# Kernel optimization log

Measured on AMD Instinct MI355X. Metric: run time of the kernel, lower is better.

## Reference

```python
import jax, jax.numpy as jnp
import numpy as np

N = 50000   # nodes
E = 600000  # edges (time_feat is per-edge: same mask indexes k and src_idx)
D = 128     # adapter_dim
C = 8       # num_clusters
SCALE = D ** -0.5


def setup_inputs() -> dict:
    key = jax.random.key(0)
    ks = jax.random.split(key, 12)
    s = 1.0 / np.sqrt(D)
    return {
        "node_feat": jax.random.normal(ks[0], (N, D), jnp.float32),
        "time_feat": jax.random.normal(ks[1], (E, D), jnp.float32),
        "context_feat": jax.random.normal(ks[2], (N, D), jnp.float32),
        "edge_index": jax.random.randint(ks[3], (2, E), 0, N),
        "Wq": jax.random.uniform(ks[4], (D, D), jnp.float32, -s, s),
        "bq": jnp.zeros((D,), jnp.float32),
        "Wk": jax.random.uniform(ks[5], (D, D), jnp.float32, -s, s),
        "bk": jnp.zeros((D,), jnp.float32),
        "Wv": jax.random.uniform(ks[6], (D, D), jnp.float32, -s, s),
        "bv": jnp.zeros((D,), jnp.float32),
        "cluster_emb": jax.random.normal(ks[7], (C, D), jnp.float32),
        "Wo": jax.random.uniform(ks[8], (D, D), jnp.float32, -s, s),
        "bo": jnp.zeros((D,), jnp.float32),
    }


def reference(node_feat, time_feat, context_feat, edge_index,
              Wq, bq, Wk, bk, Wv, bv, cluster_emb, Wo, bo):
    q = node_feat @ Wq + bq            # [N, D]
    k = time_feat @ Wk + bk            # [E, D]
    v = time_feat @ Wv + bv            # [E, D]

    # cluster routing: argmax(softmax(sim)) == argmax(sim)
    sim = (time_feat @ cluster_emb.T) * SCALE   # [E, C]
    assign = jnp.argmax(sim, axis=-1)           # [E] int

    src = edge_index[0]                          # [E]
    seg = assign * N + src                       # combined (cluster, dst-of-scatter) segment id
    nseg = C * N

    attn = jnp.sum(q[src] * k, axis=-1) * SCALE  # [E]

    # scatter_softmax per (cluster, src node)
    seg_max = jax.ops.segment_max(attn, seg, num_segments=nseg)
    ex = jnp.exp(attn - seg_max[seg])
    denom = jax.ops.segment_sum(ex, seg, num_segments=nseg)
    w = ex / denom[seg]                          # [E]

    # scatter_mean per (cluster, src node) -> [C, N, D]
    wv = v * w[:, None]
    sums = jax.ops.segment_sum(wv, seg, num_segments=nseg)                 # [C*N, D]
    counts = jax.ops.segment_sum(jnp.ones((E,), v.dtype), seg, num_segments=nseg)
    means = sums / jnp.maximum(counts, 1.0)[:, None]                       # empty -> 0
    per_cluster = means.reshape(C, N, D)

    # sum(outputs) / len(outputs): only non-empty clusters contribute an entry
    edges_per_cluster = jax.ops.segment_sum(jnp.ones((E,), jnp.float32), assign, num_segments=C)
    num_nonempty = jnp.sum((edges_per_cluster > 0).astype(jnp.float32))
    combined = per_cluster.sum(axis=0) / num_nonempty                      # [N, D]

    return jax.nn.relu(combined @ Wo + bo)
```

## Files before the change

kernel.cpp:

```cpp
#include <hip/hip_runtime.h>
#include <math.h>


#define NN 50000
#define NE 600000
#define DD 128
#define NC 8
#define WIN 64
#define NWIN 9376
#define NBF  9377
#define EC 60
#define NLOC 32
#define SCALEF 0.08838834764831845f

#define OFF_NODECNT  0
#define OFF_FILL     50000
#define OFF_MASK     100000
#define ZERO_ELEMS   100256
#define OFF_NODEOFF  100352
#define OFF_PARTIAL  150352
#define OFF_BF       150608
#define OFF_BQK      160000
#define OFF_BVO      160128
#define OFF_WQBK     160256
#define OFF_C0       160384
#define OFF_WQK      160400
#define OFF_WVO      176784
#define OFF_QB       193168
#define OFF_SORTED   243168
#define OFF_SRCS     843168
#define OFF_SW       1443168
#define OFF_P        1493168

__global__ __launch_bounds__(256) void k_pre_count(
    const float* __restrict__ Wq, const float* __restrict__ bq,
    const float* __restrict__ Wk, const float* __restrict__ bk,
    const float* __restrict__ Wv, const float* __restrict__ bv,
    const float* __restrict__ Wo, const int* __restrict__ ei,
    int* __restrict__ node_cnt,
    float* __restrict__ Wqk, float* __restrict__ bqk,
    float* __restrict__ Wvo, float* __restrict__ bvo,
    float* __restrict__ wqbk, float* __restrict__ c0) {
  int bid = blockIdx.x, t = threadIdx.x;
  if (bid >= 129) {
    long e = (long)(bid - 129) * 256 + t;
    if (e < NE) atomicAdd(&node_cnt[ei[e]], 1);
    return;
  }
  __shared__ float rq[DD], rv[DD];
  int b = bid;
  if (b < DD) {
    if (t < DD) { rq[t] = Wq[b * DD + t]; rv[t] = Wv[b * DD + t]; }
    __syncthreads();
    if (t < DD) {
      float aq = 0.f, av = 0.f;
      for (int j = 0; j < DD; j++) {
        aq += rq[j] * Wk[t * DD + j];
        av += rv[j] * Wo[j * DD + t];
      }
      Wqk[b * DD + t] = aq;
      Wvo[b * DD + t] = av;
    }
  } else {
    if (t < DD) {
      float a1 = 0.f, a2 = 0.f, a3 = 0.f;
      for (int j = 0; j < DD; j++) {
        a1 += bq[j] * Wk[t * DD + j];
        a2 += bv[j] * Wo[j * DD + t];
        a3 += Wq[t * DD + j] * bk[j];
      }
      bqk[t] = a1; bvo[t] = a2; wqbk[t] = a3;
      if (t == 0) {
        float s = 0.f;
        for (int j = 0; j < DD; j++) s += bq[j] * bk[j];
        *c0 = s;
      }
    }
  }
}

__global__ __launch_bounds__(256) void k_p(
    const float* __restrict__ nf, const float* __restrict__ Wqk,
    const float* __restrict__ bqk, const float* __restrict__ wqbk,
    const float* __restrict__ c0p,
    float* __restrict__ p, float* __restrict__ qb) {
  __shared__ float a_lds[64 * DD];
  __shared__ float wb_lds[DD];
  int t = threadIdx.x;
  long row0 = (long)blockIdx.x * 64;
  for (int it = 0; it < 8; it++) {
    int idx = (it * 256 + t) * 4;
    long r = row0 + idx / DD;
    float4 v = {0.f, 0.f, 0.f, 0.f};
    if (r < NN) v = *(const float4*)(nf + r * DD + (idx % DD));
    *(float4*)(a_lds + idx) = v;
  }
  if (t < DD) wb_lds[t] = wqbk[t];
  __syncthreads();
  int cg = t % 32, rg = t / 32;
  int col0 = cg * 4, r0 = rg * 8;
  float acc[8][4]; float qacc[8];
  for (int r = 0; r < 8; r++) { qacc[r] = 0.f; for (int c = 0; c < 4; c++) acc[r][c] = 0.f; }
  for (int k = 0; k < DD; k++) {
    float4 b4 = *(const float4*)(Wqk + k * DD + col0);
    float wbk = wb_lds[k];
    for (int r = 0; r < 8; r++) {
      float a = a_lds[(r0 + r) * DD + k];
      acc[r][0] += a * b4.x; acc[r][1] += a * b4.y;
      acc[r][2] += a * b4.z; acc[r][3] += a * b4.w;
      qacc[r] += a * wbk;
    }
  }
  float4 bq4 = *(const float4*)(bqk + col0);
  float c0v = *c0p;
  for (int r = 0; r < 8; r++) {
    long row = row0 + r0 + r;
    if (row < NN) {
      float4 o;
      o.x = acc[r][0] + bq4.x; o.y = acc[r][1] + bq4.y;
      o.z = acc[r][2] + bq4.z; o.w = acc[r][3] + bq4.w;
      *(float4*)(p + row * DD + col0) = o;
      if (cg == 0) qb[row] = qacc[r] + c0v;
    }
  }
}

__global__ __launch_bounds__(256) void k_scan1(const int* __restrict__ node_cnt,
                                               int* __restrict__ partial) {
  int i = blockIdx.x * 256 + threadIdx.x;
  int v = (i < NN) ? node_cnt[i] : 0;
  for (int o = 1; o < 64; o <<= 1) v += __shfl_xor(v, o);
  __shared__ int wsum[4];
  if ((threadIdx.x & 63) == 0) wsum[threadIdx.x >> 6] = v;
  __syncthreads();
  if (threadIdx.x == 0) partial[blockIdx.x] = wsum[0] + wsum[1] + wsum[2] + wsum[3];
}

__global__ __launch_bounds__(256) void k_scan2(int* __restrict__ partial) {
  __shared__ int s[256];
  int t = threadIdx.x;
  int v = (t < 196) ? partial[t] : 0;
  s[t] = v;
  __syncthreads();
  for (int o = 1; o < 256; o <<= 1) {
    int add = (t >= o) ? s[t - o] : 0;
    __syncthreads();
    s[t] += add;
    __syncthreads();
  }
  if (t < 196) partial[t] = s[t] - v;
}

__global__ __launch_bounds__(256) void k_scan3(const int* __restrict__ node_cnt,
                                               const int* __restrict__ partial,
                                               int* __restrict__ node_off) {
  __shared__ int s[256];
  int t = threadIdx.x;
  int i = blockIdx.x * 256 + t;
  int v = (i < NN) ? node_cnt[i] : 0;
  s[t] = v;
  __syncthreads();
  for (int o = 1; o < 256; o <<= 1) {
    int add = (t >= o) ? s[t - o] : 0;
    __syncthreads();
    s[t] += add;
    __syncthreads();
  }
  if (i < NN) node_off[i] = partial[blockIdx.x] + s[t] - v;
}

#define EDGE_BLKS 2344
#define BS_BLKS   37
__global__ __launch_bounds__(256) void k_scatter(const int* __restrict__ ei,
                                                 const int* __restrict__ node_off,
                                                 int* __restrict__ fill,
                                                 int* __restrict__ sorted,
                                                 int* __restrict__ srcs,
                                                 int* __restrict__ blockFirst) {
  int bid = blockIdx.x, t = threadIdx.x;
  if (bid >= EDGE_BLKS) {
    int w = (bid - EDGE_BLKS) * 256 + t;
    if (w < NBF) {
      int v = w * WIN, lo = 0, hi = NN;
      while (lo < hi) { int mid = (lo + hi) >> 1; if (node_off[mid] < v) lo = mid + 1; else hi = mid; }
      blockFirst[w] = lo;
    }
    return;
  }
  long e = (long)bid * 256 + t;
  if (e < NE) {
    int s = ei[e];
    int pos = node_off[s] + atomicAdd(&fill[s], 1);
    sorted[pos] = (int)e;
    srcs[pos] = s;
  }
}

__device__ __forceinline__ void phase_a(
    const float* __restrict__ tf, const float* __restrict__ p,
    const float* ce_lds, float* t_lds, float* exf_sh, int* cli_sh,
    float* D_sh, int* C_sh,
    int slot, int j, int eid, int src, int lnode, float qbv,
    bool doStage, bool doDC) {
  const float* trow = tf + (long)eid * DD;
  float4 tv[4];
  #pragma unroll
  for (int i = 0; i < 4; i++) tv[i] = *(const float4*)(trow + (i * 8 + j) * 4);
  if (doStage) {
    int e7 = slot & 7;
    #pragma unroll
    for (int i = 0; i < 4; i++)
      *(float4*)(t_lds + slot * DD + (((i * 8 + j) ^ e7) << 2)) = tv[i];
  }
  const float* prow = p + (long)src * DD;
  float a = 0.f;
  #pragma unroll
  for (int i = 0; i < 4; i++) {
    float4 pv = *(const float4*)(prow + (i * 8 + j) * 4);
    a += tv[i].x * pv.x + tv[i].y * pv.y + tv[i].z * pv.z + tv[i].w * pv.w;
  }
  float sims[NC];
  #pragma unroll
  for (int c = 0; c < NC; c++) {
    const float* cr = ce_lds + c * DD;
    float s = 0.f;
    #pragma unroll
    for (int i = 0; i < 4; i++) {
      float4 cv = *(const float4*)(cr + (i * 8 + j) * 4);
      s += tv[i].x * cv.x + tv[i].y * cv.y + tv[i].z * cv.z + tv[i].w * cv.w;
    }
    sims[c] = s;
  }
  #pragma unroll
  for (int c = 0; c < NC; c++) {
    sims[c] += __shfl_xor(sims[c], 1);
    sims[c] += __shfl_xor(sims[c], 2);
    sims[c] += __shfl_xor(sims[c], 4);
  }
  a += __shfl_xor(a, 1);
  a += __shfl_xor(a, 2);
  a += __shfl_xor(a, 4);
  if (j == 0) {
    float best = sims[0]; int bc = 0;
    #pragma unroll
    for (int c = 1; c < NC; c++) if (sims[c] > best) { best = sims[c]; bc = c; }
    float ex = expf((a + qbv) * SCALEF);
    exf_sh[slot] = ex; cli_sh[slot] = bc;
    if (doDC) {
      atomicAdd(&D_sh[lnode * NC + bc], ex);
      atomicAdd(&C_sh[lnode * NC + bc], 1);
    }
  }
}

__global__ __launch_bounds__(256) void k_fused4(
    const float* __restrict__ tf, const int* __restrict__ sorted,
    const int* __restrict__ srcs, const int* __restrict__ node_off,
    const int* __restrict__ node_cnt, const int* __restrict__ blockFirst,
    const float* __restrict__ ce, const float* __restrict__ p,
    const float* __restrict__ qb, int* __restrict__ maskArr,
    float* __restrict__ agg, float* __restrict__ sw) {
  __shared__ float t_lds[EC * DD];
  __shared__ float ce_lds[NC * DD];
  __shared__ float exf_sh[EC];
  __shared__ float scl_sh[EC];
  __shared__ int   cli_sh[EC];
  __shared__ int   offL_sh[NLOC];
  __shared__ int   cntL_sh[NLOC];
  __shared__ float qb_sh[NLOC];
  __shared__ float D_sh[NLOC * NC];
  __shared__ int   C_sh[NLOC * NC];
  __shared__ int   ctrl[4];

  int t = threadIdx.x, b = blockIdx.x;
  int fn = blockFirst[b], ln = blockFirst[b + 1] - 1;
  if (fn >= NN || ln < fn) return;

  *(float4*)(ce_lds + t * 4) = *(const float4*)(ce + t * 4);

  int el8 = t >> 3, j8 = t & 7;
  int team = t >> 5, c4 = t & 31;
  int msk = 0;

  int s0 = fn;
  while (s0 <= ln) {
    if (t < 64) {
      int offv = 0, cntv = 0; bool fit = false;
      bool valid = (t < NLOC && s0 + t <= ln);
      if (valid) { offv = node_off[s0 + t]; cntv = node_cnt[s0 + t]; }
      int off0 = __shfl(offv, 0);
      if (valid) {
        fit = (offv - off0 + cntv) <= EC;
        offL_sh[t] = offv - off0; cntL_sh[t] = cntv; qb_sh[t] = qb[s0 + t];
      }
      unsigned long long bm = __ballot(fit);
      int pref = (int)__popcll(bm);
      if (t == 0) { ctrl[0] = pref; ctrl[2] = off0; }
      if (pref > 0 && t == pref - 1) ctrl[1] = offv - off0 + cntv;
    }
    for (int i = t; i < NLOC * NC; i += 256) { D_sh[i] = 0.f; C_sh[i] = 0; }
    __syncthreads();
    int nN = ctrl[0], eb = ctrl[2];

    if (nN == 0) {
      int cnt = cntL_sh[0];
      float qbv0 = qb_sh[0];
      for (int c0 = 0; c0 < cnt; c0 += 32) {
        int el = c0 + el8;
        if (el < cnt)
          phase_a(tf, p, ce_lds, t_lds, exf_sh, cli_sh, D_sh, C_sh,
                  el8, j8, sorted[eb + el], s0, 0, qbv0, false, true);
      }
      __syncthreads();
      float4 r = {0.f, 0.f, 0.f, 0.f};
      for (int c0 = 0; c0 < cnt; c0 += EC) {
        int m = cnt - c0; if (m > EC) m = EC;
        for (int r0 = 0; r0 < m; r0 += 32) {
          int sl = r0 + el8;
          if (sl < m)
            phase_a(tf, p, ce_lds, t_lds, exf_sh, cli_sh, D_sh, C_sh,
                    sl, j8, sorted[eb + c0 + sl], s0, 0, qbv0, true, false);
        }
        __syncthreads();
        if (t < m) {
          int c = cli_sh[t];
          scl_sh[t] = exf_sh[t] * __builtin_amdgcn_rcpf(D_sh[c] * (float)C_sh[c]);
        }
        __syncthreads();
        for (int e = team; e < m; e += 8) {
          float s = scl_sh[e];
          const float4 tv = *(const float4*)(t_lds + e * DD + ((c4 ^ (e & 7)) << 2));
          r.x += s * tv.x; r.y += s * tv.y; r.z += s * tv.z; r.w += s * tv.w;
        }
        __syncthreads();
      }
      *(float4*)(t_lds + team * DD + c4 * 4) = r;
      __syncthreads();
      if (t < DD) {
        float acc = 0.f;
        #pragma unroll
        for (int tm = 0; tm < 8; tm++) acc += t_lds[tm * DD + t];
        agg[(long)s0 * DD + t] = acc;
      }
      if (t == 0) {
        float ssw = 0.f; int mk = 0;
        #pragma unroll
        for (int c = 0; c < NC; c++) {
          int cc = C_sh[c];
          if (cc > 0) { mk |= 1 << c; ssw += __builtin_amdgcn_rcpf((float)cc); }
        }
        sw[s0] = ssw; msk |= mk;
      }
      __syncthreads();
      s0 += 1;
      continue;
    }

    int span = ctrl[1];

    for (int r0 = 0; r0 < span; r0 += 32) {
      int el = r0 + el8;
      if (el < span) {
        int src = srcs[eb + el];
        phase_a(tf, p, ce_lds, t_lds, exf_sh, cli_sh, D_sh, C_sh,
                el, j8, sorted[eb + el], src, src - s0, qb_sh[src - s0],
                true, true);
      }
    }
    __syncthreads();

    if (t < span) {
      int l = (srcs[eb + t] - s0) * NC + cli_sh[t];
      scl_sh[t] = exf_sh[t] * __builtin_amdgcn_rcpf(D_sh[l] * (float)C_sh[l]);
    }
    __syncthreads();

    for (int k = team; k < nN; k += 8) {
      float4 r = {0.f, 0.f, 0.f, 0.f};
      int e1 = offL_sh[k] + cntL_sh[k];
      for (int e = offL_sh[k]; e < e1; e++) {
        float s = scl_sh[e];
        const float4 tv = *(const float4*)(t_lds + e * DD + ((c4 ^ (e & 7)) << 2));
        r.x += s * tv.x; r.y += s * tv.y; r.z += s * tv.z; r.w += s * tv.w;
      }
      long n = s0 + k;
      *(float4*)(agg + n * DD + c4 * 4) = r;
      if (c4 == 0) {
        float ssw = 0.f; int mk = 0;
        #pragma unroll
        for (int c = 0; c < NC; c++) {
          int cc = C_sh[k * NC + c];
          if (cc > 0) { mk |= 1 << c; ssw += __builtin_amdgcn_rcpf((float)cc); }
        }
        sw[n] = ssw; msk |= mk;
      }
    }
    __syncthreads();
    s0 += nN;
  }
  if ((t & 31) == 0 && msk) atomicOr(&maskArr[b & 255], msk);
}

__global__ __launch_bounds__(256) void k_out(
    const float* __restrict__ agg, const float* __restrict__ Wvo,
    const float* __restrict__ bvo, const float* __restrict__ sw,
    const float* __restrict__ bo, const int* __restrict__ maskArr,
    float* __restrict__ out) {
  __shared__ float a_lds[64 * DD];
  __shared__ float sw_lds[64];
  __shared__ int morw[4];
  int t = threadIdx.x;
  int mv = maskArr[t];
  for (int o = 1; o < 64; o <<= 1) mv |= __shfl_xor(mv, o);
  if ((t & 63) == 0) morw[t >> 6] = mv;
  long row0 = (long)blockIdx.x * 64;
  for (int it = 0; it < 8; it++) {
    int idx = (it * 256 + t) * 4;
    long r = row0 + idx / DD;
    float4 v = {0.f, 0.f, 0.f, 0.f};
    if (r < NN) v = *(const float4*)(agg + r * DD + (idx % DD));
    *(float4*)(a_lds + idx) = v;
  }
  if (t < 64) {
    long r = row0 + t;
    sw_lds[t] = (r < NN) ? sw[r] : 0.f;
  }
  __syncthreads();
  int full = morw[0] | morw[1] | morw[2] | morw[3];
  int nne = __popc(full); if (nne == 0) nne = 1;
  float inv = 1.0f / (float)nne;
  int cg = t % 32, rg = t / 32;
  int col0 = cg * 4, r0 = rg * 8;
  float acc[8][4];
  for (int r = 0; r < 8; r++) for (int c = 0; c < 4; c++) acc[r][c] = 0.f;
  for (int k = 0; k < DD; k++) {
    float4 b4 = *(const float4*)(Wvo + k * DD + col0);
    for (int r = 0; r < 8; r++) {
      float a = a_lds[(r0 + r) * DD + k];
      acc[r][0] += a * b4.x; acc[r][1] += a * b4.y;
      acc[r][2] += a * b4.z; acc[r][3] += a * b4.w;
    }
  }
  float4 bv4 = *(const float4*)(bvo + col0);
  float4 bo4 = *(const float4*)(bo + col0);
  for (int r = 0; r < 8; r++) {
    long row = row0 + r0 + r;
    if (row < NN) {
      float s = sw_lds[r0 + r];
      float4 o;
      o.x = fmaxf((acc[r][0] + s * bv4.x) * inv + bo4.x, 0.f);
      o.y = fmaxf((acc[r][1] + s * bv4.y) * inv + bo4.y, 0.f);
      o.z = fmaxf((acc[r][2] + s * bv4.z) * inv + bo4.z, 0.f);
      o.w = fmaxf((acc[r][3] + s * bv4.w) * inv + bo4.w, 0.f);
      *(float4*)(out + row * DD + col0) = o;
    }
  }
}

extern "C" void kernel_launch(void* const* d_in, const int* in_sizes, int n_in,
                              void* d_out, int out_size, void* d_ws, size_t ws_size,
                              hipStream_t stream) {
  const float* nf = (const float*)d_in[0];
  const float* tf = (const float*)d_in[1];
  const int*   ei = (const int*)d_in[3];
  const float* Wq = (const float*)d_in[4];
  const float* bq = (const float*)d_in[5];
  const float* Wk = (const float*)d_in[6];
  const float* bk = (const float*)d_in[7];
  const float* Wv = (const float*)d_in[8];
  const float* bv = (const float*)d_in[9];
  const float* ce = (const float*)d_in[10];
  const float* Wo = (const float*)d_in[11];
  const float* bo = (const float*)d_in[12];
  float* out = (float*)d_out;

  float* ws  = (float*)d_ws;
  int*   node_cnt = (int*)(ws + OFF_NODECNT);
  int*   fill     = (int*)(ws + OFF_FILL);
  int*   maskArr  = (int*)(ws + OFF_MASK);
  int*   node_off = (int*)(ws + OFF_NODEOFF);
  int*   partial  = (int*)(ws + OFF_PARTIAL);
  int*   blockFirst = (int*)(ws + OFF_BF);
  float* bqk      = ws + OFF_BQK;
  float* bvo      = ws + OFF_BVO;
  float* wqbk     = ws + OFF_WQBK;
  float* c0       = ws + OFF_C0;
  float* Wqk      = ws + OFF_WQK;
  float* Wvo      = ws + OFF_WVO;
  float* qb       = ws + OFF_QB;
  int*   sorted   = (int*)(ws + OFF_SORTED);
  int*   srcs     = (int*)(ws + OFF_SRCS);
  float* sw       = ws + OFF_SW;
  float* p        = ws + OFF_P;
  float* agg      = ws + OFF_P;

  hipMemsetAsync(d_ws, 0, (size_t)ZERO_ELEMS * 4, stream);

  k_pre_count<<<129 + EDGE_BLKS, 256, 0, stream>>>(
      Wq, bq, Wk, bk, Wv, bv, Wo, ei, node_cnt, Wqk, bqk, Wvo, bvo, wqbk, c0);
  k_p<<<(NN + 63) / 64, 256, 0, stream>>>(nf, Wqk, bqk, wqbk, c0, p, qb);
  k_scan1<<<196, 256, 0, stream>>>(node_cnt, partial);
  k_scan2<<<1, 256, 0, stream>>>(partial);
  k_scan3<<<196, 256, 0, stream>>>(node_cnt, partial, node_off);
  k_scatter<<<EDGE_BLKS + BS_BLKS, 256, 0, stream>>>(ei, node_off, fill, sorted,
                                                     srcs, blockFirst);
  k_fused4<<<NWIN, 256, 0, stream>>>(tf, sorted, srcs, node_off, node_cnt,
                                     blockFirst, ce, p, qb, maskArr, agg, sw);
  k_out<<<(NN + 63) / 64, 256, 0, stream>>>(agg, Wvo, bvo, sw, bo, maskArr, out);
}
```

Baseline: 688.7 us.

## Hold cluster embeddings in registers, use 16-lane edge groups, prefetch next edge row

The fused edge kernel now keeps each lane's slice of the cluster embeddings in registers instead of shared memory. Edges are processed 16 at a time with 16 lanes per edge instead of 32 with 8 lanes, and edge and source indices are staged in shared memory. The multi-node path software-pipelines the time-feature row loads, fetching the next edge's row while the current one is computed. EC grows from 60 to 70 and launch bounds request 4 blocks per SM. The aim is to hide global load latency and cut LDS traffic, at the cost of more registers, an extra shuffle step per reduction, and more shared memory per block.

```diff
diff --git a/kernel.cpp b/kernel.cpp
--- a/kernel.cpp
+++ b/kernel.cpp
@@ -9,7 +9,7 @@
 #define WIN 64
 #define NWIN 9376
 #define NBF  9377
-#define EC 60
+#define EC 70
 #define NLOC 32
 #define SCALEF 0.08838834764831845f
 
@@ -32,6 +32,10 @@
 #define OFF_SW       1443168
 #define OFF_P        1493168
 
+__device__ __forceinline__ float dot4(float4 a, float4 b) {
+  return a.x * b.x + a.y * b.y + a.z * b.z + a.w * b.w;
+}
+
 __global__ __launch_bounds__(256) void k_pre_count(
     const float* __restrict__ Wq, const float* __restrict__ bq,
     const float* __restrict__ Wk, const float* __restrict__ bk,
@@ -196,51 +200,40 @@
   }
 }
 
-__device__ __forceinline__ void phase_a(
+__device__ __forceinline__ void phase_a16(
     const float* __restrict__ tf, const float* __restrict__ p,
-    const float* ce_lds, float* t_lds, float* exf_sh, int* cli_sh,
+    const float4 (&ceg)[NC][2], float* t_lds, float* exf_sh, int* cli_sh,
     float* D_sh, int* C_sh,
-    int slot, int j, int eid, int src, int lnode, float qbv,
+    int slot, int jA, int eid, int src, int lnode, float qbv,
     bool doStage, bool doDC) {
   const float* trow = tf + (long)eid * DD;
-  float4 tv[4];
-  #pragma unroll
-  for (int i = 0; i < 4; i++) tv[i] = *(const float4*)(trow + (i * 8 + j) * 4);
+  float4 t0 = *(const float4*)(trow + jA * 4);
+  float4 t1 = *(const float4*)(trow + (16 + jA) * 4);
   if (doStage) {
     int e7 = slot & 7;
-    #pragma unroll
-    for (int i = 0; i < 4; i++)
-      *(float4*)(t_lds + slot * DD + (((i * 8 + j) ^ e7) << 2)) = tv[i];
+    *(float4*)(t_lds + slot * DD + ((jA ^ e7) << 2)) = t0;
+    *(float4*)(t_lds + slot * DD + ((16 + (jA ^ e7)) << 2)) = t1;
   }
   const float* prow = p + (long)src * DD;
-  float a = 0.f;
-  #pragma unroll
-  for (int i = 0; i < 4; i++) {
-    float4 pv = *(const float4*)(prow + (i * 8 + j) * 4);
-    a += tv[i].x * pv.x + tv[i].y * pv.y + tv[i].z * pv.z + tv[i].w * pv.w;
-  }
+  float4 p0 = *(const float4*)(prow + jA * 4);
+  float4 p1 = *(const float4*)(prow + (16 + jA) * 4);
+  float a = dot4(t0, p0) + dot4(t1, p1);
   float sims[NC];
   #pragma unroll
-  for (int c = 0; c < NC; c++) {
-    const float* cr = ce_lds + c * DD;
-    float s = 0.f;
-    #pragma unroll
-    for (int i = 0; i < 4; i++) {
-      float4 cv = *(const float4*)(cr + (i * 8 + j) * 4);
-      s += tv[i].x * cv.x + tv[i].y * cv.y + tv[i].z * cv.z + tv[i].w * cv.w;
-    }
-    sims[c] = s;
-  }
+  for (int c = 0; c < NC; c++)
+    sims[c] = dot4(t0, ceg[c][0]) + dot4(t1, ceg[c][1]);
   #pragma unroll
   for (int c = 0; c < NC; c++) {
     sims[c] += __shfl_xor(sims[c], 1);
     sims[c] += __shfl_xor(sims[c], 2);
     sims[c] += __shfl_xor(sims[c], 4);
+    sims[c] += __shfl_xor(sims[c], 8);
   }
   a += __shfl_xor(a, 1);
   a += __shfl_xor(a, 2);
   a += __shfl_xor(a, 4);
-  if (j == 0) {
+  a += __shfl_xor(a, 8);
+  if (jA == 0) {
     float best = sims[0]; int bc = 0;
     #pragma unroll
     for (int c = 1; c < NC; c++) if (sims[c] > best) { best = sims[c]; bc = c; }
@@ -253,7 +246,7 @@
   }
 }
 
-__global__ __launch_bounds__(256) void k_fused4(
+__global__ __launch_bounds__(256, 4) void k_fused5(
     const float* __restrict__ tf, const int* __restrict__ sorted,
     const int* __restrict__ srcs, const int* __restrict__ node_off,
     const int* __restrict__ node_cnt, const int* __restrict__ blockFirst,
@@ -261,10 +254,11 @@
     const float* __restrict__ qb, int* __restrict__ maskArr,
     float* __restrict__ agg, float* __restrict__ sw) {
   __shared__ float t_lds[EC * DD];
-  __shared__ float ce_lds[NC * DD];
   __shared__ float exf_sh[EC];
   __shared__ float scl_sh[EC];
   __shared__ int   cli_sh[EC];
+  __shared__ int   eidx_sh[EC];
+  __shared__ int   srcs_sh[EC];
   __shared__ int   offL_sh[NLOC];
   __shared__ int   cntL_sh[NLOC];
   __shared__ float qb_sh[NLOC];
@@ -276,11 +270,16 @@
   int fn = blockFirst[b], ln = blockFirst[b + 1] - 1;
   if (fn >= NN || ln < fn) return;
 
-  *(float4*)(ce_lds + t * 4) = *(const float4*)(ce + t * 4);
-
-  int el8 = t >> 3, j8 = t & 7;
+  int elA = t >> 4, jA = t & 15;
   int team = t >> 5, c4 = t & 31;
   int msk = 0;
+
+  float4 ceg[NC][2];
+  #pragma unroll
+  for (int c = 0; c < NC; c++) {
+    ceg[c][0] = *(const float4*)(ce + c * DD + jA * 4);
+    ceg[c][1] = *(const float4*)(ce + c * DD + (16 + jA) * 4);
+  }
 
   int s0 = fn;
   while (s0 <= ln) {
@@ -305,21 +304,21 @@
     if (nN == 0) {
       int cnt = cntL_sh[0];
       float qbv0 = qb_sh[0];
-      for (int c0 = 0; c0 < cnt; c0 += 32) {
-        int el = c0 + el8;
+      for (int c0 = 0; c0 < cnt; c0 += 16) {
+        int el = c0 + elA;
         if (el < cnt)
-          phase_a(tf, p, ce_lds, t_lds, exf_sh, cli_sh, D_sh, C_sh,
-                  el8, j8, sorted[eb + el], s0, 0, qbv0, false, true);
+          phase_a16(tf, p, ceg, t_lds, exf_sh, cli_sh, D_sh, C_sh,
+                    elA, jA, sorted[eb + el], s0, 0, qbv0, false, true);
       }
       __syncthreads();
       float4 r = {0.f, 0.f, 0.f, 0.f};
       for (int c0 = 0; c0 < cnt; c0 += EC) {
         int m = cnt - c0; if (m > EC) m = EC;
-        for (int r0 = 0; r0 < m; r0 += 32) {
-          int sl = r0 + el8;
+        for (int r0 = 0; r0 < m; r0 += 16) {
+          int sl = r0 + elA;
           if (sl < m)
-            phase_a(tf, p, ce_lds, t_lds, exf_sh, cli_sh, D_sh, C_sh,
-                    sl, j8, sorted[eb + c0 + sl], s0, 0, qbv0, true, false);
+            phase_a16(tf, p, ceg, t_lds, exf_sh, cli_sh, D_sh, C_sh,
+                      sl, jA, sorted[eb + c0 + sl], s0, 0, qbv0, true, false);
         }
         __syncthreads();
         if (t < m) {
@@ -358,19 +357,64 @@
 
     int span = ctrl[1];
 
-    for (int r0 = 0; r0 < span; r0 += 32) {
-      int el = r0 + el8;
+    if (t < span) { eidx_sh[t] = sorted[eb + t]; srcs_sh[t] = srcs[eb + t]; }
+    __syncthreads();
+
+    float4 tc0 = {0.f,0.f,0.f,0.f}, tc1 = {0.f,0.f,0.f,0.f};
+    if (elA < span) {
+      const float* tr = tf + (long)eidx_sh[elA] * DD;
+      tc0 = *(const float4*)(tr + jA * 4);
+      tc1 = *(const float4*)(tr + (16 + jA) * 4);
+    }
+    for (int r0 = 0; r0 < span; r0 += 16) {
+      int el = r0 + elA;
+      int eln = el + 16;
+      float4 tn0 = {0.f,0.f,0.f,0.f}, tn1 = {0.f,0.f,0.f,0.f};
+      if (eln < span) {
+        const float* tr = tf + (long)eidx_sh[eln] * DD;
+        tn0 = *(const float4*)(tr + jA * 4);
+        tn1 = *(const float4*)(tr + (16 + jA) * 4);
+      }
       if (el < span) {
-        int src = srcs[eb + el];
-        phase_a(tf, p, ce_lds, t_lds, exf_sh, cli_sh, D_sh, C_sh,
-                el, j8, sorted[eb + el], src, src - s0, qb_sh[src - s0],
-                true, true);
-      }
+        int src = srcs_sh[el];
+        int e7 = el & 7;
+        *(float4*)(t_lds + el * DD + ((jA ^ e7) << 2)) = tc0;
+        *(float4*)(t_lds + el * DD + ((16 + (jA ^ e7)) << 2)) = tc1;
+        const float* prow = p + (long)src * DD;
+        float4 p0 = *(const float4*)(prow + jA * 4);
+        float4 p1 = *(const float4*)(prow + (16 + jA) * 4);
+        float a = dot4(tc0, p0) + dot4(tc1, p1);
+        float sims[NC];
+        #pragma unroll
+        for (int c = 0; c < NC; c++)
+          sims[c] = dot4(tc0, ceg[c][0]) + dot4(tc1, ceg[c][1]);
+        #pragma unroll
+        for (int c = 0; c < NC; c++) {
+          sims[c] += __shfl_xor(sims[c], 1);
+          sims[c] += __shfl_xor(sims[c], 2);
+          sims[c] += __shfl_xor(sims[c], 4);
+          sims[c] += __shfl_xor(sims[c], 8);
+        }
+        a += __shfl_xor(a, 1);
+        a += __shfl_xor(a, 2);
+        a += __shfl_xor(a, 4);
+        a += __shfl_xor(a, 8);
+        if (jA == 0) {
+          float best = sims[0]; int bc = 0;
+          #pragma unroll
+          for (int c = 1; c < NC; c++) if (sims[c] > best) { best = sims[c]; bc = c; }
+          float ex = expf((a + qb_sh[src - s0]) * SCALEF);
+          exf_sh[el] = ex; cli_sh[el] = bc;
+          atomicAdd(&D_sh[(src - s0) * NC + bc], ex);
+          atomicAdd(&C_sh[(src - s0) * NC + bc], 1);
+        }
+      }
+      tc0 = tn0; tc1 = tn1;
     }
     __syncthreads();
 
     if (t < span) {
-      int l = (srcs[eb + t] - s0) * NC + cli_sh[t];
+      int l = (srcs_sh[t] - s0) * NC + cli_sh[t];
       scl_sh[t] = exf_sh[t] * __builtin_amdgcn_rcpf(D_sh[l] * (float)C_sh[l]);
     }
     __syncthreads();
@@ -504,7 +548,7 @@
   k_scan3<<<196, 256, 0, stream>>>(node_cnt, partial, node_off);
   k_scatter<<<EDGE_BLKS + BS_BLKS, 256, 0, stream>>>(ei, node_off, fill, sorted,
                                                      srcs, blockFirst);
-  k_fused4<<<NWIN, 256, 0, stream>>>(tf, sorted, srcs, node_off, node_cnt,
+  k_fused5<<<NWIN, 256, 0, stream>>>(tf, sorted, srcs, node_off, node_cnt,
                                      blockFirst, ce, p, qb, maskArr, agg, sw);
   k_out<<<(NN + 63) / 64, 256, 0, stream>>>(agg, Wvo, bvo, sw, bo, maskArr, out);
 }
```

New measurement: 666.0 us. 3.3% less time.

## Drop LDS staging of edge rows, enlarge windows, prefetch next edge batch

Applied to the files above, without the earlier changes.

The fused edge kernel no longer stages time_feat rows in shared memory. The aggregation phase re-reads them from global memory, relying on cache reuse, which frees a large LDS allocation so more blocks can be resident (launch bounds now request 6 blocks per SM). Windows double to 128 edges with an edge capacity of 160. Each 16-lane group handles two edges and software-prefetches the next batch of rows. The cost is that every row is read twice from global or L2 memory, with more registers used for the prefetched data.

```diff
diff --git a/kernel.cpp b/kernel.cpp
--- a/kernel.cpp
+++ b/kernel.cpp
@@ -6,10 +6,10 @@
 #define NE 600000
 #define DD 128
 #define NC 8
-#define WIN 64
-#define NWIN 9376
-#define NBF  9377
-#define EC 60
+#define WIN 128
+#define NWIN 4688
+#define NBF  4689
+#define EC 160
 #define NLOC 32
 #define SCALEF 0.08838834764831845f
 
@@ -32,6 +32,10 @@
 #define OFF_SW       1443168
 #define OFF_P        1493168
 
+__device__ __forceinline__ float dot4(float4 a, float4 b) {
+  return a.x * b.x + a.y * b.y + a.z * b.z + a.w * b.w;
+}
+
 __global__ __launch_bounds__(256) void k_pre_count(
     const float* __restrict__ Wq, const float* __restrict__ bq,
     const float* __restrict__ Wk, const float* __restrict__ bk,
@@ -170,7 +174,7 @@
 }
 
 #define EDGE_BLKS 2344
-#define BS_BLKS   37
+#define BS_BLKS   19
 __global__ __launch_bounds__(256) void k_scatter(const int* __restrict__ ei,
                                                  const int* __restrict__ node_off,
                                                  int* __restrict__ fill,
@@ -196,71 +200,41 @@
   }
 }
 
-__device__ __forceinline__ void phase_a(
+__device__ __forceinline__ void edge_ex_bc(
     const float* __restrict__ tf, const float* __restrict__ p,
-    const float* ce_lds, float* t_lds, float* exf_sh, int* cli_sh,
-    float* D_sh, int* C_sh,
-    int slot, int j, int eid, int src, int lnode, float qbv,
-    bool doStage, bool doDC) {
-  const float* trow = tf + (long)eid * DD;
-  float4 tv[4];
+    const float* ce_lds, float qbv, long eid, int src, int jA,
+    float& ex, int& bc) {
+  const float* tr = tf + eid * DD;
+  float4 t0 = *(const float4*)(tr + jA * 4);
+  float4 t1 = *(const float4*)(tr + 64 + jA * 4);
+  const float* pr = p + (long)src * DD;
+  float a = dot4(t0, *(const float4*)(pr + jA * 4)) +
+            dot4(t1, *(const float4*)(pr + 64 + jA * 4));
+  float s[NC];
   #pragma unroll
-  for (int i = 0; i < 4; i++) tv[i] = *(const float4*)(trow + (i * 8 + j) * 4);
-  if (doStage) {
-    int e7 = slot & 7;
-    #pragma unroll
-    for (int i = 0; i < 4; i++)
-      *(float4*)(t_lds + slot * DD + (((i * 8 + j) ^ e7) << 2)) = tv[i];
-  }
-  const float* prow = p + (long)src * DD;
-  float a = 0.f;
-  #pragma unroll
-  for (int i = 0; i < 4; i++) {
-    float4 pv = *(const float4*)(prow + (i * 8 + j) * 4);
-    a += tv[i].x * pv.x + tv[i].y * pv.y + tv[i].z * pv.z + tv[i].w * pv.w;
-  }
-  float sims[NC];
+  for (int c = 0; c < NC; c++)
+    s[c] = dot4(t0, *(const float4*)(ce_lds + c * DD + jA * 4)) +
+           dot4(t1, *(const float4*)(ce_lds + c * DD + 64 + jA * 4));
   #pragma unroll
   for (int c = 0; c < NC; c++) {
-    const float* cr = ce_lds + c * DD;
-    float s = 0.f;
-    #pragma unroll
-    for (int i = 0; i < 4; i++) {
-      float4 cv = *(const float4*)(cr + (i * 8 + j) * 4);
-      s += tv[i].x * cv.x + tv[i].y * cv.y + tv[i].z * cv.z + tv[i].w * cv.w;
-    }
-    sims[c] = s;
-  }
+    s[c] += __shfl_xor(s[c], 1); s[c] += __shfl_xor(s[c], 2);
+    s[c] += __shfl_xor(s[c], 4); s[c] += __shfl_xor(s[c], 8);
+  }
+  a += __shfl_xor(a, 1); a += __shfl_xor(a, 2);
+  a += __shfl_xor(a, 4); a += __shfl_xor(a, 8);
+  float best = s[0]; bc = 0;
   #pragma unroll
-  for (int c = 0; c < NC; c++) {
-    sims[c] += __shfl_xor(sims[c], 1);
-    sims[c] += __shfl_xor(sims[c], 2);
-    sims[c] += __shfl_xor(sims[c], 4);
-  }
-  a += __shfl_xor(a, 1);
-  a += __shfl_xor(a, 2);
-  a += __shfl_xor(a, 4);
-  if (j == 0) {
-    float best = sims[0]; int bc = 0;
-    #pragma unroll
-    for (int c = 1; c < NC; c++) if (sims[c] > best) { best = sims[c]; bc = c; }
-    float ex = expf((a + qbv) * SCALEF);
-    exf_sh[slot] = ex; cli_sh[slot] = bc;
-    if (doDC) {
-      atomicAdd(&D_sh[lnode * NC + bc], ex);
-      atomicAdd(&C_sh[lnode * NC + bc], 1);
-    }
-  }
-}
-
-__global__ __launch_bounds__(256) void k_fused4(
+  for (int c = 1; c < NC; c++) if (s[c] > best) { best = s[c]; bc = c; }
+  ex = expf((a + qbv) * SCALEF);
+}
+
+__global__ __launch_bounds__(256, 6) void k_fused6(
     const float* __restrict__ tf, const int* __restrict__ sorted,
     const int* __restrict__ srcs, const int* __restrict__ node_off,
     const int* __restrict__ node_cnt, const int* __restrict__ blockFirst,
     const float* __restrict__ ce, const float* __restrict__ p,
     const float* __restrict__ qb, int* __restrict__ maskArr,
     float* __restrict__ agg, float* __restrict__ sw) {
-  __shared__ float t_lds[EC * DD];
   __shared__ float ce_lds[NC * DD];
   __shared__ float exf_sh[EC];
   __shared__ float scl_sh[EC];
@@ -270,6 +244,7 @@
   __shared__ float qb_sh[NLOC];
   __shared__ float D_sh[NLOC * NC];
   __shared__ int   C_sh[NLOC * NC];
+  __shared__ float comb[8 * DD];
   __shared__ int   ctrl[4];
 
   int t = threadIdx.x, b = blockIdx.x;
@@ -278,7 +253,7 @@
 
   *(float4*)(ce_lds + t * 4) = *(const float4*)(ce + t * 4);
 
-  int el8 = t >> 3, j8 = t & 7;
+  int g = t >> 4, jA = t & 15;
   int team = t >> 5, c4 = t & 31;
   int msk = 0;
 
@@ -305,21 +280,34 @@
     if (nN == 0) {
       int cnt = cntL_sh[0];
       float qbv0 = qb_sh[0];
-      for (int c0 = 0; c0 < cnt; c0 += 32) {
-        int el = c0 + el8;
-        if (el < cnt)
-          phase_a(tf, p, ce_lds, t_lds, exf_sh, cli_sh, D_sh, C_sh,
-                  el8, j8, sorted[eb + el], s0, 0, qbv0, false, true);
+      for (int base = 0; base < cnt; base += 32) {
+        #pragma unroll
+        for (int q = 0; q < 2; q++) {
+          int e = base + 2 * g + q;
+          if (e < cnt) {
+            float ex; int bc;
+            edge_ex_bc(tf, p, ce_lds, qbv0, (long)sorted[eb + e], s0, jA, ex, bc);
+            if (jA == 0) {
+              atomicAdd(&D_sh[bc], ex);
+              atomicAdd(&C_sh[bc], 1);
+            }
+          }
+        }
       }
       __syncthreads();
       float4 r = {0.f, 0.f, 0.f, 0.f};
       for (int c0 = 0; c0 < cnt; c0 += EC) {
         int m = cnt - c0; if (m > EC) m = EC;
-        for (int r0 = 0; r0 < m; r0 += 32) {
-          int sl = r0 + el8;
-          if (sl < m)
-            phase_a(tf, p, ce_lds, t_lds, exf_sh, cli_sh, D_sh, C_sh,
-                    sl, j8, sorted[eb + c0 + sl], s0, 0, qbv0, true, false);
+        for (int base = 0; base < m; base += 32) {
+          #pragma unroll
+          for (int q = 0; q < 2; q++) {
+            int e = base + 2 * g + q;
+            if (e < m) {
+              float ex; int bc;
+              edge_ex_bc(tf, p, ce_lds, qbv0, (long)sorted[eb + c0 + e], s0, jA, ex, bc);
+              if (jA == 0) { exf_sh[e] = ex; cli_sh[e] = bc; }
+            }
+          }
         }
         __syncthreads();
         if (t < m) {
@@ -329,17 +317,17 @@
         __syncthreads();
         for (int e = team; e < m; e += 8) {
           float s = scl_sh[e];
-          const float4 tv = *(const float4*)(t_lds + e * DD + ((c4 ^ (e & 7)) << 2));
+          const float4 tv = *(const float4*)(tf + (long)sorted[eb + c0 + e] * DD + c4 * 4);
           r.x += s * tv.x; r.y += s * tv.y; r.z += s * tv.z; r.w += s * tv.w;
         }
         __syncthreads();
       }
-      *(float4*)(t_lds + team * DD + c4 * 4) = r;
+      *(float4*)(comb + team * DD + c4 * 4) = r;
       __syncthreads();
       if (t < DD) {
         float acc = 0.f;
         #pragma unroll
-        for (int tm = 0; tm < 8; tm++) acc += t_lds[tm * DD + t];
+        for (int tm = 0; tm < 8; tm++) acc += comb[tm * DD + t];
         agg[(long)s0 * DD + t] = acc;
       }
       if (t == 0) {
@@ -358,14 +346,86 @@
 
     int span = ctrl[1];
 
-    for (int r0 = 0; r0 < span; r0 += 32) {
-      int el = r0 + el8;
-      if (el < span) {
-        int src = srcs[eb + el];
-        phase_a(tf, p, ce_lds, t_lds, exf_sh, cli_sh, D_sh, C_sh,
-                el, j8, sorted[eb + el], src, src - s0, qb_sh[src - s0],
-                true, true);
-      }
+    int e0 = 2 * g, e1 = 2 * g + 1;
+    float4 ta0 = {0,0,0,0}, ta1 = {0,0,0,0}, tb0 = {0,0,0,0}, tb1 = {0,0,0,0};
+    if (e0 < span) {
+      const float* tr = tf + (long)sorted[eb + e0] * DD;
+      ta0 = *(const float4*)(tr + jA * 4);
+      ta1 = *(const float4*)(tr + 64 + jA * 4);
+    }
+    if (e1 < span) {
+      const float* tr = tf + (long)sorted[eb + e1] * DD;
+      tb0 = *(const float4*)(tr + jA * 4);
+      tb1 = *(const float4*)(tr + 64 + jA * 4);
+    }
+    for (int base = 0; base < span; base += 32) {
+      int ce0 = base + 2 * g, ce1 = ce0 + 1;
+      int ne0 = ce0 + 32, ne1 = ce1 + 32;
+      float4 na0 = {0,0,0,0}, na1 = {0,0,0,0}, nb0 = {0,0,0,0}, nb1 = {0,0,0,0};
+      if (ne0 < span) {
+        const float* tr = tf + (long)sorted[eb + ne0] * DD;
+        na0 = *(const float4*)(tr + jA * 4);
+        na1 = *(const float4*)(tr + 64 + jA * 4);
+      }
+      if (ne1 < span) {
+        const float* tr = tf + (long)sorted[eb + ne1] * DD;
+        nb0 = *(const float4*)(tr + jA * 4);
+        nb1 = *(const float4*)(tr + 64 + jA * 4);
+      }
+      int sA = 0, sB = 0;
+      float a0 = 0.f, a1 = 0.f;
+      if (ce0 < span) {
+        sA = srcs[eb + ce0];
+        const float* pr = p + (long)sA * DD;
+        a0 = dot4(ta0, *(const float4*)(pr + jA * 4)) +
+             dot4(ta1, *(const float4*)(pr + 64 + jA * 4));
+      }
+      if (ce1 < span) {
+        sB = srcs[eb + ce1];
+        const float* pr = p + (long)sB * DD;
+        a1 = dot4(tb0, *(const float4*)(pr + jA * 4)) +
+             dot4(tb1, *(const float4*)(pr + 64 + jA * 4));
+      }
+      float s0v[NC], s1v[NC];
+      #pragma unroll
+      for (int c = 0; c < NC; c++) {
+        float4 cf0 = *(const float4*)(ce_lds + c * DD + jA * 4);
+        float4 cf1 = *(const float4*)(ce_lds + c * DD + 64 + jA * 4);
+        s0v[c] = dot4(ta0, cf0) + dot4(ta1, cf1);
+        s1v[c] = dot4(tb0, cf0) + dot4(tb1, cf1);
+      }
+      #pragma unroll
+      for (int c = 0; c < NC; c++) {
+        s0v[c] += __shfl_xor(s0v[c], 1); s0v[c] += __shfl_xor(s0v[c], 2);
+        s0v[c] += __shfl_xor(s0v[c], 4); s0v[c] += __shfl_xor(s0v[c], 8);
+        s1v[c] += __shfl_xor(s1v[c], 1); s1v[c] += __shfl_xor(s1v[c], 2);
+        s1v[c] += __shfl_xor(s1v[c], 4); s1v[c] += __shfl_xor(s1v[c], 8);
+      }
+      a0 += __shfl_xor(a0, 1); a0 += __shfl_xor(a0, 2);
+      a0 += __shfl_xor(a0, 4); a0 += __shfl_xor(a0, 8);
+      a1 += __shfl_xor(a1, 1); a1 += __shfl_xor(a1, 2);
+      a1 += __shfl_xor(a1, 4); a1 += __shfl_xor(a1, 8);
+      if (jA == 0) {
+        if (ce0 < span) {
+          float best = s0v[0]; int bc = 0;
+          #pragma unroll
+          for (int c = 1; c < NC; c++) if (s0v[c] > best) { best = s0v[c]; bc = c; }
+          float ex = expf((a0 + qb_sh[sA - s0]) * SCALEF);
+          exf_sh[ce0] = ex; cli_sh[ce0] = bc;
+          atomicAdd(&D_sh[(sA - s0) * NC + bc], ex);
+          atomicAdd(&C_sh[(sA - s0) * NC + bc], 1);
+        }
+        if (ce1 < span) {
+          float best = s1v[0]; int bc = 0;
+          #pragma unroll
+          for (int c = 1; c < NC; c++) if (s1v[c] > best) { best = s1v[c]; bc = c; }
+          float ex = expf((a1 + qb_sh[sB - s0]) * SCALEF);
+          exf_sh[ce1] = ex; cli_sh[ce1] = bc;
+          atomicAdd(&D_sh[(sB - s0) * NC + bc], ex);
+          atomicAdd(&C_sh[(sB - s0) * NC + bc], 1);
+        }
+      }
+      ta0 = na0; ta1 = na1; tb0 = nb0; tb1 = nb1;
     }
     __syncthreads();
 
@@ -377,10 +437,10 @@
 
     for (int k = team; k < nN; k += 8) {
       float4 r = {0.f, 0.f, 0.f, 0.f};
-      int e1 = offL_sh[k] + cntL_sh[k];
-      for (int e = offL_sh[k]; e < e1; e++) {
+      int eS = offL_sh[k], eE = eS + cntL_sh[k];
+      for (int e = eS; e < eE; e++) {
         float s = scl_sh[e];
-        const float4 tv = *(const float4*)(t_lds + e * DD + ((c4 ^ (e & 7)) << 2));
+        const float4 tv = *(const float4*)(tf + (long)sorted[eb + e] * DD + c4 * 4);
         r.x += s * tv.x; r.y += s * tv.y; r.z += s * tv.z; r.w += s * tv.w;
       }
       long n = s0 + k;
@@ -504,7 +564,7 @@
   k_scan3<<<196, 256, 0, stream>>>(node_cnt, partial, node_off);
   k_scatter<<<EDGE_BLKS + BS_BLKS, 256, 0, stream>>>(ei, node_off, fill, sorted,
                                                      srcs, blockFirst);
-  k_fused4<<<NWIN, 256, 0, stream>>>(tf, sorted, srcs, node_off, node_cnt,
+  k_fused6<<<NWIN, 256, 0, stream>>>(tf, sorted, srcs, node_off, node_cnt,
                                      blockFirst, ce, p, qb, maskArr, agg, sw);
   k_out<<<(NN + 63) / 64, 256, 0, stream>>>(agg, Wvo, bvo, sw, bo, maskArr, out);
 }
```

Result: slower. 971.3 us (+41.0%).
